# Optimization experiments

Hardware: AMD Instinct MI355X
Metric: run time of the kernel (lower is better)

Reference implementation:

```python
import jax, jax.numpy as jnp
import numpy as np

N_NODES = 50000
N_EDGES = 800000
D = 96        # node_dim
DE = 96       # edge_dim
K_HOPS = 4
K = 2         # module's k; uses edge_attr[:, k-1]


def setup_inputs() -> dict:
    key = jax.random.key(0)
    ks = jax.random.split(key, 12)
    s = 1.0 / np.sqrt(D)
    se = 1.0 / np.sqrt(DE)
    s2 = 1.0 / np.sqrt(2 * D)
    return {
        "V": jax.random.normal(ks[0], (N_NODES, D), jnp.float32),
        "V_in": jax.random.normal(ks[1], (N_NODES, D), jnp.float32),
        "E": jax.random.normal(ks[2], (N_EDGES, DE), jnp.float32),
        "edge_attr": jax.random.uniform(ks[3], (N_EDGES, K_HOPS), jnp.float32),
        "src": jax.random.randint(ks[4], (N_EDGES,), 0, N_NODES),
        "dst": jax.random.randint(ks[5], (N_EDGES,), 0, N_NODES),
        # NodePooling linear A: node_dim -> node_dim
        "A_w": jax.random.uniform(ks[6], (D, D), jnp.float32, -s, s),
        "A_b": jax.random.uniform(ks[7], (D,), jnp.float32, -s, s),
        # M: edge_dim -> node_dim
        "M_w": jax.random.uniform(ks[8], (DE, D), jnp.float32, -se, se),
        "M_b": jax.random.uniform(ks[9], (D,), jnp.float32, -se, se),
        # W: 2*node_dim -> node_dim
        "W_w": jax.random.uniform(ks[10], (2 * D, D), jnp.float32, -s2, s2),
        "W_b": jax.random.uniform(ks[11], (D,), jnp.float32, -s2, s2),
    }


def reference(V, V_in, E, edge_attr, src, dst, A_w, A_b, M_w, M_b, W_w, W_b):
    # V = LeakyReLU(V, 0.2)
    V = jax.nn.leaky_relu(V, negative_slope=0.2)
    # NodePooling: ReLU(Linear(V))
    Vp = jax.nn.relu(V @ A_w + A_b)                      # [N, D]
    # edge projection
    Ep = E @ M_w + M_b                                   # [M, D]
    khop = edge_attr[:, K - 1:K]                         # [M, 1]
    # message: (src['V'] + data['E']) * KHOP, then sum-aggregate to dst
    msg = (Vp[src] + Ep) * khop                          # [M, D]
    agg = jax.ops.segment_sum(msg, dst, num_segments=N_NODES)  # [N, D]
    # cat aggregate with V_in, project, relu
    out = jax.nn.relu(jnp.concatenate([agg, V_in], axis=-1) @ W_w + W_b)
    return out
```

## Files before the change

### kernel.cpp

```cpp
#include <hip/hip_runtime.h>
#include <hip/hip_bf16.h>

#define NN 50000
#define NE 800000
#define DD 96
#define SVP 100
#define CAP 64

typedef float f4 __attribute__((ext_vector_type(4)));
typedef int   i4 __attribute__((ext_vector_type(4)));

__global__ __launch_bounds__(256) void k_vp(
    const float* __restrict__ V, const float* __restrict__ Aw,
    const float* __restrict__ Ab, float* __restrict__ Vp,
    int* __restrict__ cnt)
{
    __shared__ float sW[DD * DD];
    __shared__ float sV[64 * SVP];
    __shared__ float sB[DD];

    const int tid = threadIdx.x;
    const int gt = blockIdx.x * 256 + tid;
    if (gt < NN) cnt[gt] = 0;

    for (int i = tid; i < DD * DD / 4; i += 256)
        reinterpret_cast<f4*>(sW)[i] = reinterpret_cast<const f4*>(Aw)[i];
    if (tid < DD / 4)
        reinterpret_cast<f4*>(sB)[tid] = reinterpret_cast<const f4*>(Ab)[tid];

    const int row0 = blockIdx.x * 64;
    const int nr = min(64, NN - row0);
    for (int i = tid; i < nr * (DD / 4); i += 256) {
        const int r = i / (DD / 4);
        const int c = i % (DD / 4);
        f4 v = reinterpret_cast<const f4*>(V + (size_t)(row0 + r) * DD)[c];
        v[0] = v[0] > 0.f ? v[0] : 0.2f * v[0];
        v[1] = v[1] > 0.f ? v[1] : 0.2f * v[1];
        v[2] = v[2] > 0.f ? v[2] : 0.2f * v[2];
        v[3] = v[3] > 0.f ? v[3] : 0.2f * v[3];
        reinterpret_cast<f4*>(sV + r * SVP)[c] = v;
    }
    __syncthreads();

    const int cg = tid & 15;
    const int rg = tid >> 4;
    const int c0 = cg * 6;
    const int r0 = rg * 4;

    float acc[4][6];
#pragma unroll
    for (int rr = 0; rr < 4; ++rr)
#pragma unroll
        for (int j = 0; j < 6; ++j) acc[rr][j] = sB[c0 + j];

#pragma unroll 4
    for (int k = 0; k < DD; ++k) {
        float x[4];
#pragma unroll
        for (int rr = 0; rr < 4; ++rr) x[rr] = sV[(r0 + rr) * SVP + k];
#pragma unroll
        for (int j = 0; j < 6; ++j) {
            const float w = sW[k * DD + c0 + j];
#pragma unroll
            for (int rr = 0; rr < 4; ++rr)
                acc[rr][j] = fmaf(x[rr], w, acc[rr][j]);
        }
    }

#pragma unroll
    for (int rr = 0; rr < 4; ++rr) {
        const int row = row0 + r0 + rr;
        if (row < NN) {
#pragma unroll
            for (int j = 0; j < 6; ++j)
                Vp[(size_t)row * DD + c0 + j] = fmaxf(acc[rr][j], 0.f);
        }
    }
}

__global__ __launch_bounds__(256) void k_scatter(
    const int* __restrict__ src, const int* __restrict__ dst,
    const float* __restrict__ ea, int* __restrict__ cnt,
    i4* __restrict__ aux)
{
    const int e = blockIdx.x * 256 + threadIdx.x;
    if (e >= NE) return;
    const int d = dst[e];
    const int pos = atomicAdd(&cnt[d], 1);
    i4 a;
    a.x = src[e];
    a.y = e;
    a.z = __float_as_int(ea[(size_t)e * 4 + 1]);
    a.w = 0;
    if (pos < CAP)
        __builtin_nontemporal_store(a, aux + (size_t)d * CAP + pos);
}

__global__ __launch_bounds__(256) void k_aggout(
    const float* __restrict__ Vp, const float* __restrict__ E,
    const int* __restrict__ cnt, const i4* __restrict__ aux,
    const float* __restrict__ Vin, const float* __restrict__ Mw,
    const float* __restrict__ Mb, const float* __restrict__ Ww,
    const float* __restrict__ Wb, float* __restrict__ out)
{
    __shared__ float sAgg[32 * SVP];
    __shared__ float sG[32 * SVP];
    __shared__ float sW[48 * DD];
    __shared__ float sB[DD];
    __shared__ float sS[32];

    const int tid = threadIdx.x;
    const int row0 = blockIdx.x * 32;

    {
        const int grp = tid >> 5;
        const int gl = tid & 31;
        const bool act = (gl < 24);

        i4 apre[4];
        int n[4];
#pragma unroll
        for (int i = 0; i < 4; ++i) {
            const int node = row0 + grp * 4 + i;
            const bool ok = (node < NN);
            apre[i] = ok ? __builtin_nontemporal_load(aux + (size_t)node * CAP + gl)
                         : i4{0, 0, 0, 0};
            n[i] = ok ? min(cnt[node], CAP) : 0;
        }

#pragma unroll
        for (int i = 0; i < 4; ++i) {
            const int nl = grp * 4 + i;
            const int node = row0 + nl;
            if (node >= NN) break;

            f4 av = {0.f, 0.f, 0.f, 0.f};
            f4 ag = {0.f, 0.f, 0.f, 0.f};
            float wsum = 0.f;

            i4 a = apre[i];
            const int nfirst = min(n[i], 32);

            int j = 0;
            for (; j + 4 <= nfirst; j += 4) {
                const int s0 = __shfl(a.x, j + 0, 32), e0 = __shfl(a.y, j + 0, 32);
                const int s1 = __shfl(a.x, j + 1, 32), e1 = __shfl(a.y, j + 1, 32);
                const int s2 = __shfl(a.x, j + 2, 32), e2 = __shfl(a.y, j + 2, 32);
                const int s3 = __shfl(a.x, j + 3, 32), e3 = __shfl(a.y, j + 3, 32);
                const float w0 = __shfl(__int_as_float(a.z), j + 0, 32);
                const float w1 = __shfl(__int_as_float(a.z), j + 1, 32);
                const float w2 = __shfl(__int_as_float(a.z), j + 2, 32);
                const float w3 = __shfl(__int_as_float(a.z), j + 3, 32);

                f4 E0 = {0,0,0,0}, E1 = {0,0,0,0}, E2 = {0,0,0,0}, E3 = {0,0,0,0};
                f4 V0 = {0,0,0,0}, V1 = {0,0,0,0}, V2 = {0,0,0,0}, V3 = {0,0,0,0};
                if (act) {
                    E0 = __builtin_nontemporal_load(
                        reinterpret_cast<const f4*>(E + (size_t)e0 * DD) + gl);
                    E1 = __builtin_nontemporal_load(
                        reinterpret_cast<const f4*>(E + (size_t)e1 * DD) + gl);
                    E2 = __builtin_nontemporal_load(
                        reinterpret_cast<const f4*>(E + (size_t)e2 * DD) + gl);
                    E3 = __builtin_nontemporal_load(
                        reinterpret_cast<const f4*>(E + (size_t)e3 * DD) + gl);
                    V0 = *(reinterpret_cast<const f4*>(Vp + (size_t)s0 * DD) + gl);
                    V1 = *(reinterpret_cast<const f4*>(Vp + (size_t)s1 * DD) + gl);
                    V2 = *(reinterpret_cast<const f4*>(Vp + (size_t)s2 * DD) + gl);
                    V3 = *(reinterpret_cast<const f4*>(Vp + (size_t)s3 * DD) + gl);
                }
#pragma unroll
                for (int c = 0; c < 4; ++c) {
                    av[c] = fmaf(w0, V0[c], av[c]);
                    av[c] = fmaf(w1, V1[c], av[c]);
                    av[c] = fmaf(w2, V2[c], av[c]);
                    av[c] = fmaf(w3, V3[c], av[c]);
                    ag[c] = fmaf(w0, E0[c], ag[c]);
                    ag[c] = fmaf(w1, E1[c], ag[c]);
                    ag[c] = fmaf(w2, E2[c], ag[c]);
                    ag[c] = fmaf(w3, E3[c], ag[c]);
                }
                wsum += w0 + w1 + w2 + w3;
            }
            for (; j < nfirst; ++j) {
                const int s0 = __shfl(a.x, j, 32), e0 = __shfl(a.y, j, 32);
                const float w0 = __shfl(__int_as_float(a.z), j, 32);
                f4 E0 = {0,0,0,0}, V0 = {0,0,0,0};
                if (act) {
                    E0 = __builtin_nontemporal_load(
                        reinterpret_cast<const f4*>(E + (size_t)e0 * DD) + gl);
                    V0 = *(reinterpret_cast<const f4*>(Vp + (size_t)s0 * DD) + gl);
                }
#pragma unroll
                for (int c = 0; c < 4; ++c) {
                    av[c] = fmaf(w0, V0[c], av[c]);
                    ag[c] = fmaf(w0, E0[c], ag[c]);
                }
                wsum += w0;
            }

            if (n[i] > 32) {
                i4 a2 = __builtin_nontemporal_load(
                    aux + (size_t)node * CAP + 32 + gl);
                const int rem = n[i] - 32;
                for (int jj = 0; jj < rem; ++jj) {
                    const int s0 = __shfl(a2.x, jj, 32), e0 = __shfl(a2.y, jj, 32);
                    const float w0 = __shfl(__int_as_float(a2.z), jj, 32);
                    f4 E0 = {0,0,0,0}, V0 = {0,0,0,0};
                    if (act) {
                        E0 = __builtin_nontemporal_load(
                            reinterpret_cast<const f4*>(E + (size_t)e0 * DD) + gl);
                        V0 = *(reinterpret_cast<const f4*>(Vp + (size_t)s0 * DD) + gl);
                    }
#pragma unroll
                    for (int c = 0; c < 4; ++c) {
                        av[c] = fmaf(w0, V0[c], av[c]);
                        ag[c] = fmaf(w0, E0[c], ag[c]);
                    }
                    wsum += w0;
                }
            }

            if (act) {
                *reinterpret_cast<f4*>(sAgg + nl * SVP + gl * 4) = av;
                *reinterpret_cast<f4*>(sG + nl * SVP + gl * 4) = ag;
            }
            if (gl == 0) sS[nl] = wsum;
        }
    }
    __syncthreads();

    const int cg = tid & 15;
    const int rg = tid >> 4;
    const int c0 = cg * 6;
    const int r0 = rg * 2;

    auto loadW = [&](const float* wsrc) {
        for (int i = tid; i < 48 * DD / 4; i += 256)
            reinterpret_cast<f4*>(sW)[i] = reinterpret_cast<const f4*>(wsrc)[i];
    };
    auto loadB = [&](const float* bsrc) {
        if (tid < DD / 4)
            reinterpret_cast<f4*>(sB)[tid] = reinterpret_cast<const f4*>(bsrc)[tid];
    };

    loadW(Mw); loadB(Mb);
    __syncthreads();

    float a[2][6];
#pragma unroll
    for (int rr = 0; rr < 2; ++rr) {
        const float sv = sS[r0 + rr];
#pragma unroll
        for (int j = 0; j < 6; ++j)
            a[rr][j] = sAgg[(r0 + rr) * SVP + c0 + j] + sv * sB[c0 + j];
    }
#pragma unroll 4
    for (int k = 0; k < 48; ++k) {
        const float x0 = sG[r0 * SVP + k];
        const float x1 = sG[(r0 + 1) * SVP + k];
#pragma unroll
        for (int j = 0; j < 6; ++j) {
            const float w = sW[k * DD + c0 + j];
            a[0][j] = fmaf(x0, w, a[0][j]);
            a[1][j] = fmaf(x1, w, a[1][j]);
        }
    }
    __syncthreads();
    loadW(Mw + 48 * DD);
    __syncthreads();
#pragma unroll 4
    for (int k = 0; k < 48; ++k) {
        const float x0 = sG[r0 * SVP + 48 + k];
        const float x1 = sG[(r0 + 1) * SVP + 48 + k];
#pragma unroll
        for (int j = 0; j < 6; ++j) {
            const float w = sW[k * DD + c0 + j];
            a[0][j] = fmaf(x0, w, a[0][j]);
            a[1][j] = fmaf(x1, w, a[1][j]);
        }
    }
#pragma unroll
    for (int rr = 0; rr < 2; ++rr)
#pragma unroll
        for (int j = 0; j < 6; ++j)
            sAgg[(r0 + rr) * SVP + c0 + j] = a[rr][j];
    __syncthreads();

    loadW(Ww); loadB(Wb);
    __syncthreads();

    float o[2][6];
#pragma unroll
    for (int rr = 0; rr < 2; ++rr)
#pragma unroll
        for (int j = 0; j < 6; ++j) o[rr][j] = sB[c0 + j];
#pragma unroll 4
    for (int k = 0; k < 48; ++k) {
        const float x0 = sAgg[r0 * SVP + k];
        const float x1 = sAgg[(r0 + 1) * SVP + k];
#pragma unroll
        for (int j = 0; j < 6; ++j) {
            const float w = sW[k * DD + c0 + j];
            o[0][j] = fmaf(x0, w, o[0][j]);
            o[1][j] = fmaf(x1, w, o[1][j]);
        }
    }
    __syncthreads();
    loadW(Ww + 48 * DD);
    __syncthreads();
#pragma unroll 4
    for (int k = 0; k < 48; ++k) {
        const float x0 = sAgg[r0 * SVP + 48 + k];
        const float x1 = sAgg[(r0 + 1) * SVP + 48 + k];
#pragma unroll
        for (int j = 0; j < 6; ++j) {
            const float w = sW[k * DD + c0 + j];
            o[0][j] = fmaf(x0, w, o[0][j]);
            o[1][j] = fmaf(x1, w, o[1][j]);
        }
    }
    __syncthreads();

    loadW(Ww + 96 * DD);
    {
        const int nr = min(32, NN - row0);
        for (int i = tid; i < nr * (DD / 4); i += 256) {
            const int r = i / (DD / 4);
            const int c = i % (DD / 4);
            reinterpret_cast<f4*>(sG + r * SVP)[c] =
                reinterpret_cast<const f4*>(Vin + (size_t)(row0 + r) * DD)[c];
        }
    }
    __syncthreads();
#pragma unroll 4
    for (int k = 0; k < 48; ++k) {
        const float x0 = sG[r0 * SVP + k];
        const float x1 = sG[(r0 + 1) * SVP + k];
#pragma unroll
        for (int j = 0; j < 6; ++j) {
            const float w = sW[k * DD + c0 + j];
            o[0][j] = fmaf(x0, w, o[0][j]);
            o[1][j] = fmaf(x1, w, o[1][j]);
        }
    }
    __syncthreads();
    loadW(Ww + 144 * DD);
    __syncthreads();
#pragma unroll 4
    for (int k = 0; k < 48; ++k) {
        const float x0 = sG[r0 * SVP + 48 + k];
        const float x1 = sG[(r0 + 1) * SVP + 48 + k];
#pragma unroll
        for (int j = 0; j < 6; ++j) {
            const float w = sW[k * DD + c0 + j];
            o[0][j] = fmaf(x0, w, o[0][j]);
            o[1][j] = fmaf(x1, w, o[1][j]);
        }
    }

#pragma unroll
    for (int rr = 0; rr < 2; ++rr) {
        const int row = row0 + r0 + rr;
        if (row < NN) {
#pragma unroll
            for (int j = 0; j < 6; ++j)
                out[(size_t)row * DD + c0 + j] = fmaxf(o[rr][j], 0.f);
        }
    }
}

extern "C" void kernel_launch(void* const* d_in, const int* in_sizes, int n_in,
                              void* d_out, int out_size, void* d_ws, size_t ws_size,
                              hipStream_t stream)
{
    const float* V   = (const float*)d_in[0];
    const float* Vin = (const float*)d_in[1];
    const float* E   = (const float*)d_in[2];
    const float* ea  = (const float*)d_in[3];
    const int*   src = (const int*)d_in[4];
    const int*   dst = (const int*)d_in[5];
    const float* Aw  = (const float*)d_in[6];
    const float* Ab  = (const float*)d_in[7];
    const float* Mw  = (const float*)d_in[8];
    const float* Mb  = (const float*)d_in[9];
    const float* Ww  = (const float*)d_in[10];
    const float* Wb  = (const float*)d_in[11];
    float* out = (float*)d_out;

    float* Vp  = (float*)d_ws;
    int*   cnt = (int*)(Vp + (size_t)NN * DD);
    size_t aux_off = (size_t)NN * DD + NN;
    aux_off = (aux_off + 3) & ~(size_t)3;
    i4*    aux = (i4*)((float*)d_ws + aux_off);

    k_vp<<<(NN + 63) / 64, 256, 0, stream>>>(V, Aw, Ab, Vp, cnt);
    k_scatter<<<(NE + 255) / 256, 256, 0, stream>>>(src, dst, ea, cnt, aux);
    k_aggout<<<(NN + 31) / 32, 256, 0, stream>>>(Vp, E, cnt, aux, Vin,
                                                 Mw, Mb, Ww, Wb, out);
}
```

Measured before the change: 246.1 us.

## Shrink weight tile, unroll gather by 8, and add occupancy launch bound

The aggregation/output kernel now stages weights in 32-row chunks instead of 48, which cuts shared memory per block, and adds __launch_bounds__(256,4) to allow more resident blocks. The gather loop gets an 8-wide unrolled stage that issues eight E and Vp row loads before accumulating, so more loads are in flight. The Vin staging is moved earlier so the weight and input loads are reorganised. Costs are more barriers from the extra weight chunks and possible register pressure or spills under the tighter launch bound.

```diff
diff --git a/kernel.cpp b/kernel.cpp
--- a/kernel.cpp
+++ b/kernel.cpp
@@ -96,7 +96,7 @@
         __builtin_nontemporal_store(a, aux + (size_t)d * CAP + pos);
 }
 
-__global__ __launch_bounds__(256) void k_aggout(
+__global__ __launch_bounds__(256, 4) void k_aggout(
     const float* __restrict__ Vp, const float* __restrict__ E,
     const int* __restrict__ cnt, const i4* __restrict__ aux,
     const float* __restrict__ Vin, const float* __restrict__ Mw,
@@ -105,7 +105,7 @@
 {
     __shared__ float sAgg[32 * SVP];
     __shared__ float sG[32 * SVP];
-    __shared__ float sW[48 * DD];
+    __shared__ float sW[32 * DD];
     __shared__ float sB[DD];
     __shared__ float sS[32];
 
@@ -142,49 +142,72 @@
             const int nfirst = min(n[i], 32);
 
             int j = 0;
+            for (; j + 8 <= nfirst; j += 8) {
+                int ss[8], ee[8];
+                float ww[8];
+#pragma unroll
+                for (int q = 0; q < 8; ++q) {
+                    ss[q] = __shfl(a.x, j + q, 32);
+                    ee[q] = __shfl(a.y, j + q, 32);
+                    ww[q] = __shfl(__int_as_float(a.z), j + q, 32);
+                }
+                f4 Ev[8], Vv[8];
+#pragma unroll
+                for (int q = 0; q < 8; ++q) {
+                    if (act) {
+                        Ev[q] = __builtin_nontemporal_load(
+                            reinterpret_cast<const f4*>(E + (size_t)ee[q] * DD) + gl);
+                        Vv[q] = *(reinterpret_cast<const f4*>(Vp + (size_t)ss[q] * DD) + gl);
+                    } else {
+                        Ev[q] = f4{0, 0, 0, 0};
+                        Vv[q] = f4{0, 0, 0, 0};
+                    }
+                }
+#pragma unroll
+                for (int q = 0; q < 8; ++q) {
+#pragma unroll
+                    for (int c = 0; c < 4; ++c) {
+                        av[c] = fmaf(ww[q], Vv[q][c], av[c]);
+                        ag[c] = fmaf(ww[q], Ev[q][c], ag[c]);
+                    }
+                    wsum += ww[q];
+                }
+            }
             for (; j + 4 <= nfirst; j += 4) {
-                const int s0 = __shfl(a.x, j + 0, 32), e0 = __shfl(a.y, j + 0, 32);
-                const int s1 = __shfl(a.x, j + 1, 32), e1 = __shfl(a.y, j + 1, 32);
-                const int s2 = __shfl(a.x, j + 2, 32), e2 = __shfl(a.y, j + 2, 32);
-                const int s3 = __shfl(a.x, j + 3, 32), e3 = __shfl(a.y, j + 3, 32);
-                const float w0 = __shfl(__int_as_float(a.z), j + 0, 32);
-                const float w1 = __shfl(__int_as_float(a.z), j + 1, 32);
-                const float w2 = __shfl(__int_as_float(a.z), j + 2, 32);
-                const float w3 = __shfl(__int_as_float(a.z), j + 3, 32);
-
-                f4 E0 = {0,0,0,0}, E1 = {0,0,0,0}, E2 = {0,0,0,0}, E3 = {0,0,0,0};
-                f4 V0 = {0,0,0,0}, V1 = {0,0,0,0}, V2 = {0,0,0,0}, V3 = {0,0,0,0};
-                if (act) {
-                    E0 = __builtin_nontemporal_load(
-                        reinterpret_cast<const f4*>(E + (size_t)e0 * DD) + gl);
-                    E1 = __builtin_nontemporal_load(
-                        reinterpret_cast<const f4*>(E + (size_t)e1 * DD) + gl);
-                    E2 = __builtin_nontemporal_load(
-                        reinterpret_cast<const f4*>(E + (size_t)e2 * DD) + gl);
-                    E3 = __builtin_nontemporal_load(
-                        reinterpret_cast<const f4*>(E + (size_t)e3 * DD) + gl);
-                    V0 = *(reinterpret_cast<const f4*>(Vp + (size_t)s0 * DD) + gl);
-                    V1 = *(reinterpret_cast<const f4*>(Vp + (size_t)s1 * DD) + gl);
-                    V2 = *(reinterpret_cast<const f4*>(Vp + (size_t)s2 * DD) + gl);
-                    V3 = *(reinterpret_cast<const f4*>(Vp + (size_t)s3 * DD) + gl);
-                }
-#pragma unroll
-                for (int c = 0; c < 4; ++c) {
-                    av[c] = fmaf(w0, V0[c], av[c]);
-                    av[c] = fmaf(w1, V1[c], av[c]);
-                    av[c] = fmaf(w2, V2[c], av[c]);
-                    av[c] = fmaf(w3, V3[c], av[c]);
-                    ag[c] = fmaf(w0, E0[c], ag[c]);
-                    ag[c] = fmaf(w1, E1[c], ag[c]);
-                    ag[c] = fmaf(w2, E2[c], ag[c]);
-                    ag[c] = fmaf(w3, E3[c], ag[c]);
-                }
-                wsum += w0 + w1 + w2 + w3;
+                int ss[4], ee[4];
+                float ww[4];
+#pragma unroll
+                for (int q = 0; q < 4; ++q) {
+                    ss[q] = __shfl(a.x, j + q, 32);
+                    ee[q] = __shfl(a.y, j + q, 32);
+                    ww[q] = __shfl(__int_as_float(a.z), j + q, 32);
+                }
+                f4 Ev[4], Vv[4];
+#pragma unroll
+                for (int q = 0; q < 4; ++q) {
+                    if (act) {
+                        Ev[q] = __builtin_nontemporal_load(
+                            reinterpret_cast<const f4*>(E + (size_t)ee[q] * DD) + gl);
+                        Vv[q] = *(reinterpret_cast<const f4*>(Vp + (size_t)ss[q] * DD) + gl);
+                    } else {
+                        Ev[q] = f4{0, 0, 0, 0};
+                        Vv[q] = f4{0, 0, 0, 0};
+                    }
+                }
+#pragma unroll
+                for (int q = 0; q < 4; ++q) {
+#pragma unroll
+                    for (int c = 0; c < 4; ++c) {
+                        av[c] = fmaf(ww[q], Vv[q][c], av[c]);
+                        ag[c] = fmaf(ww[q], Ev[q][c], ag[c]);
+                    }
+                    wsum += ww[q];
+                }
             }
             for (; j < nfirst; ++j) {
                 const int s0 = __shfl(a.x, j, 32), e0 = __shfl(a.y, j, 32);
                 const float w0 = __shfl(__int_as_float(a.z), j, 32);
-                f4 E0 = {0,0,0,0}, V0 = {0,0,0,0};
+                f4 E0 = {0, 0, 0, 0}, V0 = {0, 0, 0, 0};
                 if (act) {
                     E0 = __builtin_nontemporal_load(
                         reinterpret_cast<const f4*>(E + (size_t)e0 * DD) + gl);
@@ -205,7 +228,7 @@
                 for (int jj = 0; jj < rem; ++jj) {
                     const int s0 = __shfl(a2.x, jj, 32), e0 = __shfl(a2.y, jj, 32);
                     const float w0 = __shfl(__int_as_float(a2.z), jj, 32);
-                    f4 E0 = {0,0,0,0}, V0 = {0,0,0,0};
+                    f4 E0 = {0, 0, 0, 0}, V0 = {0, 0, 0, 0};
                     if (act) {
                         E0 = __builtin_nontemporal_load(
                             reinterpret_cast<const f4*>(E + (size_t)e0 * DD) + gl);
@@ -235,7 +258,7 @@
     const int r0 = rg * 2;
 
     auto loadW = [&](const float* wsrc) {
-        for (int i = tid; i < 48 * DD / 4; i += 256)
+        for (int i = tid; i < 32 * DD / 4; i += 256)
             reinterpret_cast<f4*>(sW)[i] = reinterpret_cast<const f4*>(wsrc)[i];
     };
     auto loadB = [&](const float* bsrc) {
@@ -254,76 +277,36 @@
         for (int j = 0; j < 6; ++j)
             a[rr][j] = sAgg[(r0 + rr) * SVP + c0 + j] + sv * sB[c0 + j];
     }
+#pragma unroll
+    for (int ch = 0; ch < 3; ++ch) {
+        if (ch) {
+            __syncthreads();
+            loadW(Mw + ch * 32 * DD);
+            __syncthreads();
+        }
+        const int kb = ch * 32;
 #pragma unroll 4
-    for (int k = 0; k < 48; ++k) {
-        const float x0 = sG[r0 * SVP + k];
-        const float x1 = sG[(r0 + 1) * SVP + k];
-#pragma unroll
-        for (int j = 0; j < 6; ++j) {
-            const float w = sW[k * DD + c0 + j];
-            a[0][j] = fmaf(x0, w, a[0][j]);
-            a[1][j] = fmaf(x1, w, a[1][j]);
+        for (int k = 0; k < 32; ++k) {
+            const float x0 = sG[r0 * SVP + kb + k];
+            const float x1 = sG[(r0 + 1) * SVP + kb + k];
+#pragma unroll
+            for (int j = 0; j < 6; ++j) {
+                const float w = sW[k * DD + c0 + j];
+                a[0][j] = fmaf(x0, w, a[0][j]);
+                a[1][j] = fmaf(x1, w, a[1][j]);
+            }
         }
     }
     __syncthreads();
-    loadW(Mw + 48 * DD);
-    __syncthreads();
-#pragma unroll 4
-    for (int k = 0; k < 48; ++k) {
-        const float x0 = sG[r0 * SVP + 48 + k];
-        const float x1 = sG[(r0 + 1) * SVP + 48 + k];
-#pragma unroll
-        for (int j = 0; j < 6; ++j) {
-            const float w = sW[k * DD + c0 + j];
-            a[0][j] = fmaf(x0, w, a[0][j]);
-            a[1][j] = fmaf(x1, w, a[1][j]);
-        }
-    }
 #pragma unroll
     for (int rr = 0; rr < 2; ++rr)
 #pragma unroll
         for (int j = 0; j < 6; ++j)
             sAgg[(r0 + rr) * SVP + c0 + j] = a[rr][j];
-    __syncthreads();
-
-    loadW(Ww); loadB(Wb);
-    __syncthreads();
-
-    float o[2][6];
-#pragma unroll
-    for (int rr = 0; rr < 2; ++rr)
-#pragma unroll
-        for (int j = 0; j < 6; ++j) o[rr][j] = sB[c0 + j];
-#pragma unroll 4
-    for (int k = 0; k < 48; ++k) {
-        const float x0 = sAgg[r0 * SVP + k];
-        const float x1 = sAgg[(r0 + 1) * SVP + k];
-#pragma unroll
-        for (int j = 0; j < 6; ++j) {
-            const float w = sW[k * DD + c0 + j];
-            o[0][j] = fmaf(x0, w, o[0][j]);
-            o[1][j] = fmaf(x1, w, o[1][j]);
-        }
-    }
-    __syncthreads();
-    loadW(Ww + 48 * DD);
-    __syncthreads();
-#pragma unroll 4
-    for (int k = 0; k < 48; ++k) {
-        const float x0 = sAgg[r0 * SVP + 48 + k];
-        const float x1 = sAgg[(r0 + 1) * SVP + 48 + k];
-#pragma unroll
-        for (int j = 0; j < 6; ++j) {
-            const float w = sW[k * DD + c0 + j];
-            o[0][j] = fmaf(x0, w, o[0][j]);
-            o[1][j] = fmaf(x1, w, o[1][j]);
-        }
-    }
-    __syncthreads();
-
-    loadW(Ww + 96 * DD);
+
     {
         const int nr = min(32, NN - row0);
+        __syncthreads();
         for (int i = tid; i < nr * (DD / 4); i += 256) {
             const int r = i / (DD / 4);
             const int c = i % (DD / 4);
@@ -331,30 +314,52 @@
                 reinterpret_cast<const f4*>(Vin + (size_t)(row0 + r) * DD)[c];
         }
     }
+
+    loadW(Ww); loadB(Wb);
     __syncthreads();
+
+    float o[2][6];
+#pragma unroll
+    for (int rr = 0; rr < 2; ++rr)
+#pragma unroll
+        for (int j = 0; j < 6; ++j) o[rr][j] = sB[c0 + j];
+#pragma unroll
+    for (int ch = 0; ch < 3; ++ch) {
+        if (ch) {
+            __syncthreads();
+            loadW(Ww + ch * 32 * DD);
+            __syncthreads();
+        }
+        const int kb = ch * 32;
 #pragma unroll 4
-    for (int k = 0; k < 48; ++k) {
-        const float x0 = sG[r0 * SVP + k];
-        const float x1 = sG[(r0 + 1) * SVP + k];
-#pragma unroll
-        for (int j = 0; j < 6; ++j) {
-            const float w = sW[k * DD + c0 + j];
-            o[0][j] = fmaf(x0, w, o[0][j]);
-            o[1][j] = fmaf(x1, w, o[1][j]);
-        }
-    }
-    __syncthreads();
-    loadW(Ww + 144 * DD);
-    __syncthreads();
+        for (int k = 0; k < 32; ++k) {
+            const float x0 = sAgg[r0 * SVP + kb + k];
+            const float x1 = sAgg[(r0 + 1) * SVP + kb + k];
+#pragma unroll
+            for (int j = 0; j < 6; ++j) {
+                const float w = sW[k * DD + c0 + j];
+                o[0][j] = fmaf(x0, w, o[0][j]);
+                o[1][j] = fmaf(x1, w, o[1][j]);
+            }
+        }
+    }
+
+#pragma unroll
+    for (int ch = 0; ch < 3; ++ch) {
+        __syncthreads();
+        loadW(Ww + (size_t)(96 + ch * 32) * DD);
+        __syncthreads();
+        const int kb = ch * 32;
 #pragma unroll 4
-    for (int k = 0; k < 48; ++k) {
-        const float x0 = sG[r0 * SVP + 48 + k];
-        const float x1 = sG[(r0 + 1) * SVP + 48 + k];
-#pragma unroll
-        for (int j = 0; j < 6; ++j) {
-            const float w = sW[k * DD + c0 + j];
-            o[0][j] = fmaf(x0, w, o[0][j]);
-            o[1][j] = fmaf(x1, w, o[1][j]);
+        for (int k = 0; k < 32; ++k) {
+            const float x0 = sG[r0 * SVP + kb + k];
+            const float x1 = sG[(r0 + 1) * SVP + kb + k];
+#pragma unroll
+            for (int j = 0; j < 6; ++j) {
+                const float w = sW[k * DD + c0 + j];
+                o[0][j] = fmaf(x0, w, o[0][j]);
+                o[1][j] = fmaf(x1, w, o[1][j]);
+            }
         }
     }
 
```

Measured after the change: 226.9 us. 7.8% less time.
